# Performance work log

Hardware: AMD Instinct MI355X
Metric: run time of the kernel (lower is better)

The kernel has to match this reference:

```python
import jax, jax.numpy as jnp
import numpy as np

B, T, DIN, D = 8, 2048, 512, 1024
LN_EPS = 1e-5


def setup_inputs() -> dict:
    key = jax.random.key(0)
    ks = jax.random.split(key, 4)
    x = jax.random.normal(ks[0], (B, T, DIN), dtype=jnp.float32)
    Wd = jax.random.normal(ks[1], (DIN, D), dtype=jnp.float32) * (1.0 / np.sqrt(DIN))
    bd = jnp.zeros((D,), jnp.float32)  # nn.init.constant_(delta_proj.bias, 0)
    Wb = jax.random.normal(ks[2], (DIN, D), dtype=jnp.float32) * (1.0 / np.sqrt(DIN))
    bb = jax.random.normal(ks[3], (D,), dtype=jnp.float32) * 0.02
    A_log = jnp.log(jnp.linspace(1.0, 16.0, D, dtype=jnp.float32))
    threshold = jnp.ones((D,), jnp.float32)
    gamma = jnp.ones((D,), jnp.float32)
    beta = jnp.zeros((D,), jnp.float32)
    return {"x": x, "Wd": Wd, "bd": bd, "Wb": Wb, "bb": bb,
            "A_log": A_log, "threshold": threshold, "gamma": gamma, "beta": beta}


def reference(x, Wd, bd, Wb, bb, A_log, threshold, gamma, beta):
    # Input-dependent discretization (parallel over B,T)
    delta = jax.nn.softplus(jnp.einsum('btc,cd->btd', x, Wd) + bd)   # [B,T,D]
    b_step = delta * (jnp.einsum('btc,cd->btd', x, Wb) + bb)          # [B,T,D]
    A = jnp.exp(A_log)                                                # [D]
    a_step = jnp.exp(-delta * A)                                      # [B,T,D]

    # Sequential spiking scan with multiplicative threshold reset (fp32)
    def step(h, ab):
        a, b = ab
        h = a * h + b
        s = (h - threshold > 0).astype(h.dtype)  # spike (no grad path)
        h = h * (1.0 - s)                        # reset
        return h, (h, s)

    aT = jnp.swapaxes(a_step, 0, 1)  # [T,B,D]
    bT = jnp.swapaxes(b_step, 0, 1)
    h0 = jnp.zeros((x.shape[0], A.shape[0]), a_step.dtype)
    _, (hT, sT) = jax.lax.scan(step, h0, (aT, bT))
    h_post = jnp.swapaxes(hT, 0, 1)  # [B,T,D]
    spikes = jnp.swapaxes(sT, 0, 1)

    # LayerNorm over last dim (biased variance, as torch)
    mu = jnp.mean(h_post, axis=-1, keepdims=True)
    var = jnp.mean(jnp.square(h_post - mu), axis=-1, keepdims=True)
    out = (h_post - mu) * jax.lax.rsqrt(var + LN_EPS) * gamma + beta
    return out, spikes
```

## Files before the change

### kernel.cpp

```cpp
#include <hip/hip_runtime.h>
#include <math.h>

#define BB   8
#define TT   2048
#define CIN  512
#define DD   1024
#define MM   (BB * TT)

constexpr int BM = 128;
constexpr int BN = 64;
constexpr int BK = 16;

#define NCHUNK 64
#define CLEN   (TT / NCHUNK)
#define WARM   64
#define PF     8

__device__ __forceinline__ void lgkm_bar() {
    asm volatile("s_waitcnt lgkmcnt(0)" ::: "memory");
    __builtin_amdgcn_s_barrier();
}

__device__ __forceinline__ float softplus_f(float z) {
    return fmaxf(z, 0.f) + log1pf(expf(-fabsf(z)));
}

__global__ __launch_bounds__(256) void k1_gemm_act(
    const float* __restrict__ x,
    const float* __restrict__ Wd,
    const float* __restrict__ Wb,
    const float* __restrict__ bd,
    const float* __restrict__ bb,
    const float* __restrict__ A_log,
    float* __restrict__ a_out,
    float* __restrict__ b_out)
{
    __shared__ float xs[BK][BM + 4];
    __shared__ float wds[BK][BN];
    __shared__ float wbs[BK][BN];

    const int tid = threadIdx.x;
    const int n0  = blockIdx.x * BN;
    const int m0  = blockIdx.y * BM;
    const int tx  = tid & 15;
    const int ty  = tid >> 4;

    const int lm = tid >> 1;
    const int lk = (tid & 1) * 8;
    const int wr = tid >> 4;
    const int wc = (tid & 15) * 4;

    float accd[8][4], accb[8][4];
#pragma unroll
    for (int r = 0; r < 8; ++r)
#pragma unroll
        for (int c = 0; c < 4; ++c) { accd[r][c] = 0.f; accb[r][c] = 0.f; }

    const float* xp  = x + (size_t)(m0 + lm) * CIN + lk;
    const float* wdp = Wd + (size_t)wr * DD + n0 + wc;
    const float* wbp = Wb + (size_t)wr * DD + n0 + wc;
    float4 xva = *(const float4*)(xp);
    float4 xvb = *(const float4*)(xp + 4);
    float4 wd0 = *(const float4*)(wdp);
    float4 wb0 = *(const float4*)(wbp);

    for (int k0 = 0; k0 < CIN; k0 += BK) {
        __syncthreads();
        xs[lk + 0][lm] = xva.x;  xs[lk + 1][lm] = xva.y;
        xs[lk + 2][lm] = xva.z;  xs[lk + 3][lm] = xva.w;
        xs[lk + 4][lm] = xvb.x;  xs[lk + 5][lm] = xvb.y;
        xs[lk + 6][lm] = xvb.z;  xs[lk + 7][lm] = xvb.w;
        *(float4*)&wds[wr][wc] = wd0;
        *(float4*)&wbs[wr][wc] = wb0;
        __syncthreads();

        const int kn = k0 + BK;
        if (kn < CIN) {
            xva = *(const float4*)(xp + kn);
            xvb = *(const float4*)(xp + kn + 4);
            wd0 = *(const float4*)(wdp + (size_t)kn * DD);
            wb0 = *(const float4*)(wbp + (size_t)kn * DD);
        }

#pragma unroll
        for (int kk = 0; kk < BK; ++kk) {
            float4 xa  = *(const float4*)&xs[kk][ty * 8];
            float4 xa2 = *(const float4*)&xs[kk][ty * 8 + 4];
            float4 d0  = *(const float4*)&wds[kk][tx * 4];
            float4 c0  = *(const float4*)&wbs[kk][tx * 4];
            float xr[8] = {xa.x, xa.y, xa.z, xa.w, xa2.x, xa2.y, xa2.z, xa2.w};
            float wd[4] = {d0.x, d0.y, d0.z, d0.w};
            float wb[4] = {c0.x, c0.y, c0.z, c0.w};
#pragma unroll
            for (int r = 0; r < 8; ++r) {
                const float xi = xr[r];
#pragma unroll
                for (int c = 0; c < 4; ++c) {
                    accd[r][c] = fmaf(xi, wd[c], accd[r][c]);
                    accb[r][c] = fmaf(xi, wb[c], accb[r][c]);
                }
            }
        }
    }

    const int nc0 = n0 + tx * 4;
    float4 bdq = *(const float4*)(bd + nc0);
    float4 bbq = *(const float4*)(bb + nc0);
    float4 alq = *(const float4*)(A_log + nc0);
    const float* bdv = (const float*)&bdq;
    const float* bbv = (const float*)&bbq;
    float Aq[4] = {expf(alq.x), expf(alq.y), expf(alq.z), expf(alq.w)};

#pragma unroll
    for (int r = 0; r < 8; ++r) {
        const int m = m0 + ty * 8 + r;
        float av[4], bv[4];
#pragma unroll
        for (int j = 0; j < 4; ++j) {
            float zd    = accd[r][j] + bdv[j];
            float delta = softplus_f(zd);
            float zb    = accb[r][j] + bbv[j];
            av[j] = expf(-delta * Aq[j]);
            bv[j] = delta * zb;
        }
        *(float4*)(a_out + (size_t)m * DD + nc0) = make_float4(av[0], av[1], av[2], av[3]);
        *(float4*)(b_out + (size_t)m * DD + nc0) = make_float4(bv[0], bv[1], bv[2], bv[3]);
    }
}


#define PREFETCH(AV, BV)                                                  \
    {                                                                     \
        _Pragma("unroll")                                                 \
        for (int j = 0; j < PF; ++j) {                                    \
            AV[j] = *(const float2*)(ap + (size_t)j * DD);                \
            BV[j] = *(const float2*)(bp + (size_t)j * DD);                \
        }                                                                 \
        ap += (size_t)PF * DD; bp += (size_t)PF * DD;                     \
    }

#define WARM_SLOT(AV, BV)                                                 \
    {                                                                     \
        _Pragma("unroll")                                                 \
        for (int j = 0; j < PF; ++j) {                                    \
            h.x = fmaf(AV[j].x, h.x, BV[j].x);                            \
            h.y = fmaf(AV[j].y, h.y, BV[j].y);                            \
            h.x = ((h.x - th.x) > 0.f) ? 0.f : h.x;                       \
            h.y = ((h.y - th.y) > 0.f) ? 0.f : h.y;                       \
        }                                                                 \
    }

#define OUT_SLOT(AV, BV, PFOK)                                            \
    {                                                                     \
        float2 hj[PF];                                                    \
        _Pragma("unroll")                                                 \
        for (int j = 0; j < PF; ++j) {                                    \
            h.x = fmaf(AV[j].x, h.x, BV[j].x);                            \
            h.y = fmaf(AV[j].y, h.y, BV[j].y);                            \
            const bool kx = (h.x - th.x) > 0.f;                           \
            const bool ky = (h.y - th.y) > 0.f;                           \
            *(float2*)(sp + (size_t)j * DD) =                             \
                make_float2(kx ? 1.f : 0.f, ky ? 1.f : 0.f);              \
            h.x = kx ? 0.f : h.x;                                         \
            h.y = ky ? 0.f : h.y;                                         \
            hj[j] = h;                                                    \
        }                                                                 \
        sp += (size_t)PF * DD;                                            \
        _Pragma("unroll")                                                 \
        for (int j = 0; j < PF; ++j) {                                    \
            trans[tid][j]      = hj[j].x + hj[j].y;                       \
            trans[tid][j + PF] = fmaf(hj[j].x, hj[j].x,                   \
                                      hj[j].y * hj[j].y);                 \
        }                                                                 \
        if (PFOK) PREFETCH(AV, BV)                                        \
        lgkm_bar();                                                       \
        {                                                                 \
            float p = 0.f;                                                \
            _Pragma("unroll")                                             \
            for (int i2 = 0; i2 < 16; ++i2)                               \
                p += trans[i2 * 32 + rs][rq];                             \
            p += __shfl_down(p, 16);                                      \
            p += __shfl_down(p, 8);                                       \
            p += __shfl_down(p, 4);                                       \
            p += __shfl_down(p, 2);                                       \
            p += __shfl_down(p, 1);                                       \
            if (rs == 0) red[rq] = p;                                     \
        }                                                                 \
        lgkm_bar();                                                       \
        float mu_[PF], inv_[PF];                                          \
        _Pragma("unroll")                                                 \
        for (int j = 0; j < PF; ++j) {                                    \
            const float mu  = red[j] * (1.0f / DD);                       \
            const float var =                                             \
                fmaxf(red[j + PF] * (1.0f / DD) - mu * mu, 0.f);          \
            mu_[j]  = mu;                                                 \
            inv_[j] = 1.0f / sqrtf(var + 1e-5f);                          \
        }                                                                 \
        _Pragma("unroll")                                                 \
        for (int j = 0; j < PF; ++j) {                                    \
            float2 o;                                                     \
            o.x = (hj[j].x - mu_[j]) * inv_[j] * g.x + be.x;              \
            o.y = (hj[j].y - mu_[j]) * inv_[j] * g.y + be.y;              \
            *(float2*)(op + (size_t)j * DD) = o;                          \
        }                                                                 \
        op += (size_t)PF * DD;                                            \
    }

__global__ __launch_bounds__(512) void k23_scan_ln(
    const float* __restrict__ a,
    const float* __restrict__ b,
    const float* __restrict__ thr,
    const float* __restrict__ gamma,
    const float* __restrict__ beta,
    float* __restrict__ out,
    float* __restrict__ spikes)
{
    const int tid   = threadIdx.x;
    const int d0    = tid * 2;
    const int chunk = blockIdx.x;
    const int batch = blockIdx.y;
    const int rq    = tid >> 5;
    const int rs    = tid & 31;

    const float2 th = *(const float2*)(thr + d0);
    const float2 g  = *(const float2*)(gamma + d0);
    const float2 be = *(const float2*)(beta + d0);

    const int t0    = chunk * CLEN;
    const int nwarm = (t0 < WARM) ? t0 : WARM;
    const int tw    = t0 - nwarm;
    const int nwb   = nwarm / PF;
    const int ntot  = nwb + CLEN / PF;

    const size_t rowbase = (size_t)batch * TT * DD + d0;
    const float* ap = a + rowbase + (size_t)tw * DD;
    const float* bp = b + rowbase + (size_t)tw * DD;
    float* op = out    + rowbase + (size_t)t0 * DD;
    float* sp = spikes + rowbase + (size_t)t0 * DD;

    __shared__ float trans[512][17];
    __shared__ float red[2 * PF];

    float2 a0[PF], b0[PF], a1[PF], b1[PF];
    PREFETCH(a0, b0)
    PREFETCH(a1, b1)

    float2 h = make_float2(0.f, 0.f);
    for (int i = 0; i < ntot; i += 2) {
        if (i >= nwb) OUT_SLOT(a0, b0, i + 2 < ntot)
        else { WARM_SLOT(a0, b0) PREFETCH(a0, b0) }

        if (i + 1 >= nwb) OUT_SLOT(a1, b1, i + 3 < ntot)
        else { WARM_SLOT(a1, b1) PREFETCH(a1, b1) }
    }
}

extern "C" void kernel_launch(void* const* d_in, const int* in_sizes, int n_in,
                              void* d_out, int out_size, void* d_ws, size_t ws_size,
                              hipStream_t stream) {
    const float* x     = (const float*)d_in[0];
    const float* Wd    = (const float*)d_in[1];
    const float* bd    = (const float*)d_in[2];
    const float* Wb    = (const float*)d_in[3];
    const float* bb    = (const float*)d_in[4];
    const float* A_log = (const float*)d_in[5];
    const float* thr   = (const float*)d_in[6];
    const float* gamma = (const float*)d_in[7];
    const float* beta  = (const float*)d_in[8];

    float* out    = (float*)d_out;
    float* spikes = out + (size_t)MM * DD;
    float* a_ws   = (float*)d_ws;
    float* b_ws   = a_ws + (size_t)MM * DD;

    dim3 g1(DD / BN, MM / BM);
    k1_gemm_act<<<g1, 256, 0, stream>>>(x, Wd, Wb, bd, bb, A_log, a_ws, b_ws);

    dim3 g2(NCHUNK, BB);
    k23_scan_ln<<<g2, 512, 0, stream>>>(a_ws, b_ws, thr, gamma, beta, out, spikes);
}
```

Measured before the change: 671.1 us.

## Batch LayerNorm reduction over two prefetch slots and halve scan chunk count

The fused scan+LayerNorm kernel now scans two 8-step slots before a single shared-memory reduction, so 16 timesteps share one pair of barriers instead of 8. The transpose buffer widens to 33 columns and the reduction uses 16-lane groups. The chunk count drops from 64 to 32, which doubles chunk length and halves the redundant 64-step warm-up relative to useful work, at the cost of fewer blocks (256) for parallelism. Register pressure rises because two hj arrays stay live.

```diff
diff --git a/kernel.cpp b/kernel.cpp
--- a/kernel.cpp
+++ b/kernel.cpp
@@ -11,7 +11,7 @@
 constexpr int BN = 64;
 constexpr int BK = 16;
 
-#define NCHUNK 64
+#define NCHUNK 32
 #define CLEN   (TT / NCHUNK)
 #define WARM   64
 #define PF     8
@@ -150,9 +150,8 @@
         }                                                                 \
     }
 
-#define OUT_SLOT(AV, BV, PFOK)                                            \
-    {                                                                     \
-        float2 hj[PF];                                                    \
+#define SCAN_SLOT(AV, BV, HJ, C0)                                         \
+    {                                                                     \
         _Pragma("unroll")                                                 \
         for (int j = 0; j < PF; ++j) {                                    \
             h.x = fmaf(AV[j].x, h.x, BV[j].x);                            \
@@ -163,23 +162,46 @@
                 make_float2(kx ? 1.f : 0.f, ky ? 1.f : 0.f);              \
             h.x = kx ? 0.f : h.x;                                         \
             h.y = ky ? 0.f : h.y;                                         \
-            hj[j] = h;                                                    \
+            HJ[j] = h;                                                    \
         }                                                                 \
         sp += (size_t)PF * DD;                                            \
         _Pragma("unroll")                                                 \
         for (int j = 0; j < PF; ++j) {                                    \
-            trans[tid][j]      = hj[j].x + hj[j].y;                       \
-            trans[tid][j + PF] = fmaf(hj[j].x, hj[j].x,                   \
-                                      hj[j].y * hj[j].y);                 \
-        }                                                                 \
-        if (PFOK) PREFETCH(AV, BV)                                        \
+            trans[tid][(C0) + j]      = HJ[j].x + HJ[j].y;                \
+            trans[tid][(C0) + j + PF] = fmaf(HJ[j].x, HJ[j].x,            \
+                                             HJ[j].y * HJ[j].y);          \
+        }                                                                 \
+    }
+
+#define LN_WRITE(HJ, RB)                                                  \
+    {                                                                     \
+        _Pragma("unroll")                                                 \
+        for (int j = 0; j < PF; ++j) {                                    \
+            const float mu  = red[(RB) + j] * (1.0f / DD);                \
+            const float var =                                             \
+                fmaxf(red[(RB) + j + PF] * (1.0f / DD) - mu * mu, 0.f);   \
+            const float inv = 1.0f / sqrtf(var + 1e-5f);                  \
+            float2 o;                                                     \
+            o.x = (HJ[j].x - mu) * inv * g.x + be.x;                      \
+            o.y = (HJ[j].y - mu) * inv * g.y + be.y;                      \
+            *(float2*)(op + (size_t)j * DD) = o;                          \
+        }                                                                 \
+        op += (size_t)PF * DD;                                            \
+    }
+
+#define OUT_PAIR(PFOK)                                                    \
+    {                                                                     \
+        float2 hj0[PF], hj1[PF];                                          \
+        SCAN_SLOT(a0, b0, hj0, 0)                                         \
+        if (PFOK) PREFETCH(a0, b0)                                        \
+        SCAN_SLOT(a1, b1, hj1, 16)                                        \
+        if (PFOK) PREFETCH(a1, b1)                                        \
         lgkm_bar();                                                       \
         {                                                                 \
             float p = 0.f;                                                \
             _Pragma("unroll")                                             \
-            for (int i2 = 0; i2 < 16; ++i2)                               \
-                p += trans[i2 * 32 + rs][rq];                             \
-            p += __shfl_down(p, 16);                                      \
+            for (int i2 = 0; i2 < 32; ++i2)                               \
+                p += trans[i2 * 16 + rs][rq];                             \
             p += __shfl_down(p, 8);                                       \
             p += __shfl_down(p, 4);                                       \
             p += __shfl_down(p, 2);                                       \
@@ -187,23 +209,8 @@
             if (rs == 0) red[rq] = p;                                     \
         }                                                                 \
         lgkm_bar();                                                       \
-        float mu_[PF], inv_[PF];                                          \
-        _Pragma("unroll")                                                 \
-        for (int j = 0; j < PF; ++j) {                                    \
-            const float mu  = red[j] * (1.0f / DD);                       \
-            const float var =                                             \
-                fmaxf(red[j + PF] * (1.0f / DD) - mu * mu, 0.f);          \
-            mu_[j]  = mu;                                                 \
-            inv_[j] = 1.0f / sqrtf(var + 1e-5f);                          \
-        }                                                                 \
-        _Pragma("unroll")                                                 \
-        for (int j = 0; j < PF; ++j) {                                    \
-            float2 o;                                                     \
-            o.x = (hj[j].x - mu_[j]) * inv_[j] * g.x + be.x;              \
-            o.y = (hj[j].y - mu_[j]) * inv_[j] * g.y + be.y;              \
-            *(float2*)(op + (size_t)j * DD) = o;                          \
-        }                                                                 \
-        op += (size_t)PF * DD;                                            \
+        LN_WRITE(hj0, 0)                                                  \
+        LN_WRITE(hj1, 16)                                                 \
     }
 
 __global__ __launch_bounds__(512) void k23_scan_ln(
@@ -219,8 +226,8 @@
     const int d0    = tid * 2;
     const int chunk = blockIdx.x;
     const int batch = blockIdx.y;
-    const int rq    = tid >> 5;
-    const int rs    = tid & 31;
+    const int rq    = tid >> 4;
+    const int rs    = tid & 15;
 
     const float2 th = *(const float2*)(thr + d0);
     const float2 g  = *(const float2*)(gamma + d0);
@@ -238,8 +245,8 @@
     float* op = out    + rowbase + (size_t)t0 * DD;
     float* sp = spikes + rowbase + (size_t)t0 * DD;
 
-    __shared__ float trans[512][17];
-    __shared__ float red[2 * PF];
+    __shared__ float trans[512][33];
+    __shared__ float red[32];
 
     float2 a0[PF], b0[PF], a1[PF], b1[PF];
     PREFETCH(a0, b0)
@@ -247,11 +254,12 @@
 
     float2 h = make_float2(0.f, 0.f);
     for (int i = 0; i < ntot; i += 2) {
-        if (i >= nwb) OUT_SLOT(a0, b0, i + 2 < ntot)
-        else { WARM_SLOT(a0, b0) PREFETCH(a0, b0) }
-
-        if (i + 1 >= nwb) OUT_SLOT(a1, b1, i + 3 < ntot)
-        else { WARM_SLOT(a1, b1) PREFETCH(a1, b1) }
+        if (i >= nwb) {
+            OUT_PAIR(i + 2 < ntot)
+        } else {
+            WARM_SLOT(a0, b0) PREFETCH(a0, b0)
+            WARM_SLOT(a1, b1) PREFETCH(a1, b1)
+        }
     }
 }
 
```

Measured after the change: 638.5 us. 1.05x faster.

## Interleave a/b workspace into one array and halve scan chunk count

Applied to the files above, without the earlier changes.

The GEMM epilogue now writes a and b interleaved per channel pair into a single workspace, so the scan kernel fetches both with one float4 load per timestep instead of two float2 loads. The scan grid also drops from 64 to 32 chunks per batch, which cuts the redundant warm-up recomputation in half. The cost is 256 blocks instead of 512, so there is less parallelism to hide the serial scan latency on a GPU with many CUs.

```diff
diff --git a/kernel.cpp b/kernel.cpp
--- a/kernel.cpp
+++ b/kernel.cpp
@@ -11,7 +11,7 @@
 constexpr int BN = 64;
 constexpr int BK = 16;
 
-#define NCHUNK 64
+#define NCHUNK 32
 #define CLEN   (TT / NCHUNK)
 #define WARM   64
 #define PF     8
@@ -32,8 +32,7 @@
     const float* __restrict__ bd,
     const float* __restrict__ bb,
     const float* __restrict__ A_log,
-    float* __restrict__ a_out,
-    float* __restrict__ b_out)
+    float* __restrict__ ab_out)
 {
     __shared__ float xs[BK][BM + 4];
     __shared__ float wds[BK][BN];
@@ -123,40 +122,39 @@
             av[j] = expf(-delta * Aq[j]);
             bv[j] = delta * zb;
         }
-        *(float4*)(a_out + (size_t)m * DD + nc0) = make_float4(av[0], av[1], av[2], av[3]);
-        *(float4*)(b_out + (size_t)m * DD + nc0) = make_float4(bv[0], bv[1], bv[2], bv[3]);
-    }
-}
-
-
-#define PREFETCH(AV, BV)                                                  \
+        float* abp = ab_out + (size_t)m * (2 * DD) + 2 * nc0;
+        *(float4*)(abp)     = make_float4(av[0], av[1], bv[0], bv[1]);
+        *(float4*)(abp + 4) = make_float4(av[2], av[3], bv[2], bv[3]);
+    }
+}
+
+
+#define PREFETCH(ABV)                                                     \
     {                                                                     \
         _Pragma("unroll")                                                 \
-        for (int j = 0; j < PF; ++j) {                                    \
-            AV[j] = *(const float2*)(ap + (size_t)j * DD);                \
-            BV[j] = *(const float2*)(bp + (size_t)j * DD);                \
-        }                                                                 \
-        ap += (size_t)PF * DD; bp += (size_t)PF * DD;                     \
-    }
-
-#define WARM_SLOT(AV, BV)                                                 \
+        for (int j = 0; j < PF; ++j)                                      \
+            ABV[j] = *(const float4*)(abp + (size_t)j * (2 * DD));        \
+        abp += (size_t)PF * (2 * DD);                                     \
+    }
+
+#define WARM_SLOT(ABV)                                                    \
     {                                                                     \
         _Pragma("unroll")                                                 \
         for (int j = 0; j < PF; ++j) {                                    \
-            h.x = fmaf(AV[j].x, h.x, BV[j].x);                            \
-            h.y = fmaf(AV[j].y, h.y, BV[j].y);                            \
+            h.x = fmaf(ABV[j].x, h.x, ABV[j].z);                          \
+            h.y = fmaf(ABV[j].y, h.y, ABV[j].w);                          \
             h.x = ((h.x - th.x) > 0.f) ? 0.f : h.x;                       \
             h.y = ((h.y - th.y) > 0.f) ? 0.f : h.y;                       \
         }                                                                 \
     }
 
-#define OUT_SLOT(AV, BV, PFOK)                                            \
+#define OUT_SLOT(ABV, PFOK)                                               \
     {                                                                     \
         float2 hj[PF];                                                    \
         _Pragma("unroll")                                                 \
         for (int j = 0; j < PF; ++j) {                                    \
-            h.x = fmaf(AV[j].x, h.x, BV[j].x);                            \
-            h.y = fmaf(AV[j].y, h.y, BV[j].y);                            \
+            h.x = fmaf(ABV[j].x, h.x, ABV[j].z);                          \
+            h.y = fmaf(ABV[j].y, h.y, ABV[j].w);                          \
             const bool kx = (h.x - th.x) > 0.f;                           \
             const bool ky = (h.y - th.y) > 0.f;                           \
             *(float2*)(sp + (size_t)j * DD) =                             \
@@ -172,7 +170,7 @@
             trans[tid][j + PF] = fmaf(hj[j].x, hj[j].x,                   \
                                       hj[j].y * hj[j].y);                 \
         }                                                                 \
-        if (PFOK) PREFETCH(AV, BV)                                        \
+        if (PFOK) PREFETCH(ABV)                                           \
         lgkm_bar();                                                       \
         {                                                                 \
             float p = 0.f;                                                \
@@ -207,8 +205,7 @@
     }
 
 __global__ __launch_bounds__(512) void k23_scan_ln(
-    const float* __restrict__ a,
-    const float* __restrict__ b,
+    const float* __restrict__ ab,
     const float* __restrict__ thr,
     const float* __restrict__ gamma,
     const float* __restrict__ beta,
@@ -232,26 +229,26 @@
     const int nwb   = nwarm / PF;
     const int ntot  = nwb + CLEN / PF;
 
+    const float* abp = ab + (size_t)batch * TT * (2 * DD)
+                          + (size_t)tw * (2 * DD) + 4 * tid;
     const size_t rowbase = (size_t)batch * TT * DD + d0;
-    const float* ap = a + rowbase + (size_t)tw * DD;
-    const float* bp = b + rowbase + (size_t)tw * DD;
     float* op = out    + rowbase + (size_t)t0 * DD;
     float* sp = spikes + rowbase + (size_t)t0 * DD;
 
     __shared__ float trans[512][17];
     __shared__ float red[2 * PF];
 
-    float2 a0[PF], b0[PF], a1[PF], b1[PF];
-    PREFETCH(a0, b0)
-    PREFETCH(a1, b1)
+    float4 ab0[PF], ab1[PF];
+    PREFETCH(ab0)
+    PREFETCH(ab1)
 
     float2 h = make_float2(0.f, 0.f);
     for (int i = 0; i < ntot; i += 2) {
-        if (i >= nwb) OUT_SLOT(a0, b0, i + 2 < ntot)
-        else { WARM_SLOT(a0, b0) PREFETCH(a0, b0) }
-
-        if (i + 1 >= nwb) OUT_SLOT(a1, b1, i + 3 < ntot)
-        else { WARM_SLOT(a1, b1) PREFETCH(a1, b1) }
+        if (i >= nwb) OUT_SLOT(ab0, i + 2 < ntot)
+        else { WARM_SLOT(ab0) PREFETCH(ab0) }
+
+        if (i + 1 >= nwb) OUT_SLOT(ab1, i + 3 < ntot)
+        else { WARM_SLOT(ab1) PREFETCH(ab1) }
     }
 }
 
@@ -270,12 +267,11 @@
 
     float* out    = (float*)d_out;
     float* spikes = out + (size_t)MM * DD;
-    float* a_ws   = (float*)d_ws;
-    float* b_ws   = a_ws + (size_t)MM * DD;
+    float* ab_ws  = (float*)d_ws;
 
     dim3 g1(DD / BN, MM / BM);
-    k1_gemm_act<<<g1, 256, 0, stream>>>(x, Wd, Wb, bd, bb, A_log, a_ws, b_ws);
+    k1_gemm_act<<<g1, 256, 0, stream>>>(x, Wd, Wb, bd, bb, A_log, ab_ws);
 
     dim3 g2(NCHUNK, BB);
-    k23_scan_ln<<<g2, 512, 0, stream>>>(a_ws, b_ws, thr, gamma, beta, out, spikes);
-}
+    k23_scan_ln<<<g2, 512, 0, stream>>>(ab_ws, thr, gamma, beta, out, spikes);
+}
```

Result: faster. 635.0 us (-5.4%).
